# Optimization experiments

Hardware: AMD Instinct MI355X
Metric: run time of the kernel (lower is better)

## Reference

```python
import jax, jax.numpy as jnp
import numpy as np

N_NODES = 100000
N_EDGES = 1600000
D_IN = 64
D_OUT = 64


def setup_inputs() -> dict:
    key = jax.random.key(0)
    k1, k2, k3, k4, k5, k6 = jax.random.split(key, 6)
    feat = jax.random.normal(k1, (N_NODES, D_IN), dtype=jnp.float32)
    src = jax.random.randint(k2, (N_EDGES,), 0, N_NODES, dtype=jnp.int64)
    dst = jax.random.randint(k3, (N_EDGES,), 0, N_NODES, dtype=jnp.int64)
    edge_weight = jax.random.uniform(k4, (N_EDGES,), dtype=jnp.float32)
    # Xavier-uniform with relu gain, as in reset_parameters
    gain = float(np.sqrt(2.0))
    bound = gain * float(np.sqrt(6.0 / (D_IN + D_OUT)))
    W_neigh = jax.random.uniform(k5, (D_OUT, D_IN), dtype=jnp.float32, minval=-bound, maxval=bound)
    W_self = jax.random.uniform(k6, (D_OUT, D_IN), dtype=jnp.float32, minval=-bound, maxval=bound)
    bias = jnp.zeros((D_OUT,), dtype=jnp.float32)
    return {"feat": feat, "src": src, "dst": dst, "edge_weight": edge_weight,
            "W_neigh": W_neigh, "W_self": W_self, "bias": bias}


def reference(feat, src, dst, edge_weight, W_neigh, W_self, bias):
    n = feat.shape[0]
    # feat_drop with p=0.0 is identity; in_feats == out_feats so lin_before_mp is False
    # message: u_mul_e -> gather src features, scale by edge weight  [E, D_IN]
    m = feat[src] * edge_weight[:, None]
    # mean reduce over incoming edges (zero for isolated dst nodes, matching DGL)
    s = jax.ops.segment_sum(m, dst, num_segments=n)
    deg = jax.ops.segment_sum(jnp.ones_like(edge_weight), dst, num_segments=n)
    neigh = s / jnp.maximum(deg, 1.0)[:, None]
    h_neigh = neigh @ W_neigh.T
    h_self = feat @ W_self.T
    return h_self + h_neigh + bias
```

## Files before the change

kernel.cpp:

```cpp
#include <hip/hip_runtime.h>

constexpr int N_NODES = 100000;
constexpr int N_EDGES = 1600000;
constexpr int D = 64;

constexpr int BSH    = 6;
constexpr int BN     = 1 << BSH;
constexpr int NBUCK  = (N_NODES + BN - 1) / BN;
constexpr int NPART  = 400;
constexpr int EPB    = N_EDGES / NPART;
constexpr int NCVT   = (N_NODES * D / 4) / 256;

constexpr size_t OFF_BCNT    = 0;
constexpr size_t OFF_CURSOR  = 8192;
constexpr size_t OFF_BSTART  = 16384;
constexpr size_t OFF_ENTRIES = 24576;
constexpr size_t OFF_W16     = 24576 + (size_t)N_EDGES * 8;
constexpr size_t OFF_FEAT16  = OFF_W16 + 32768;
constexpr size_t OFF_ENT2    = OFF_FEAT16 + (size_t)N_NODES * D * 2;
constexpr size_t OFF_NSTART  = OFF_ENT2 + (size_t)N_EDGES * 8;
constexpr size_t WS_NEEDED   = OFF_NSTART + ((size_t)NBUCK * BN + 1) * 4;

typedef short  bf16x8 __attribute__((ext_vector_type(8)));
typedef float  f32x4  __attribute__((ext_vector_type(4)));

__device__ __forceinline__ unsigned short f2bf(float f) {
    unsigned u = __float_as_uint(f);
    u += 0x7fffu + ((u >> 16) & 1u);
    return (unsigned short)(u >> 16);
}

__device__ __forceinline__ void split8(float4 p0, float4 p1, bf16x8& hi, bf16x8& lo) {
    float f[8] = {p0.x, p0.y, p0.z, p0.w, p1.x, p1.y, p1.z, p1.w};
#pragma unroll
    for (int i = 0; i < 8; ++i) {
        const unsigned short h = f2bf(f[i]);
        const float hf = __uint_as_float((unsigned)h << 16);
        hi[i] = (short)h;
        lo[i] = (short)f2bf(f[i] - hf);
    }
}

__global__ __launch_bounds__(256) void k_zero(int* __restrict__ bcnt) {
    int i = blockIdx.x * 256 + threadIdx.x;
    if (i < NBUCK) bcnt[i] = 0;
}

__global__ __launch_bounds__(256) void k_pre(const float4* __restrict__ feat4,
                                             unsigned short* __restrict__ feat16,
                                             const float* __restrict__ Wn,
                                             const float* __restrict__ Ws,
                                             unsigned short* __restrict__ W16,
                                             const int* __restrict__ dst,
                                             int* __restrict__ bcnt) {
    __shared__ int l[NBUCK];
    const int b   = blockIdx.x;
    const int tid = threadIdx.x;
    if (b < NCVT) {
        const int i = b * 256 + tid;
        float4 v = feat4[i];
        ushort4 o;
        o.x = f2bf(v.x); o.y = f2bf(v.y); o.z = f2bf(v.z); o.w = f2bf(v.w);
        *(ushort4*)&feat16[(size_t)i * 4] = o;
    } else if (b < NCVT + NPART) {
        const int base = (b - NCVT) * EPB;
        for (int i = tid; i < NBUCK; i += 256) l[i] = 0;
        __syncthreads();
        for (int k = tid; k < EPB; k += 256)
            atomicAdd(&l[dst[base + k] >> BSH], 1);
        __syncthreads();
        for (int i = tid; i < NBUCK; i += 256)
            if (l[i]) atomicAdd(&bcnt[i], l[i]);
    } else {
        for (int e = tid; e < D * 128; e += 256) {
            const int j = e >> 7, k = e & 127;
            const float w = (k < D) ? Ws[j * D + k] : Wn[j * D + (k - D)];
            const unsigned short h = f2bf(w);
            const float hf = __uint_as_float((unsigned)h << 16);
            W16[e] = h;
            W16[D * 128 + e] = f2bf(w - hf);
        }
    }
}

__global__ __launch_bounds__(1024) void k_scan(const int* __restrict__ bcnt,
                                               int* __restrict__ bstart,
                                               int* __restrict__ cursor) {
    __shared__ int s[1024];
    const int t  = threadIdx.x;
    const int i0 = 2 * t, i1 = 2 * t + 1;
    const int c0 = (i0 < NBUCK) ? bcnt[i0] : 0;
    const int c1 = (i1 < NBUCK) ? bcnt[i1] : 0;
    const int v  = c0 + c1;
    s[t] = v;
    __syncthreads();
    for (int off = 1; off < 1024; off <<= 1) {
        int u = (t >= off) ? s[t - off] : 0;
        __syncthreads();
        s[t] += u;
        __syncthreads();
    }
    const int excl = s[t] - v;
    if (i0 < NBUCK) { bstart[i0] = excl;      cursor[i0] = excl; }
    if (i1 < NBUCK) { bstart[i1] = excl + c0; cursor[i1] = excl + c0; }
    if (t == 0) bstart[NBUCK] = N_EDGES;
}

__global__ __launch_bounds__(256) void k_part(const int* __restrict__ src,
                                              const int* __restrict__ dst,
                                              const float* __restrict__ ew,
                                              int* __restrict__ cursor,
                                              uint2* __restrict__ entries) {
    __shared__ int l[NBUCK];
    const int tid  = threadIdx.x;
    const int base = blockIdx.x * EPB;
    for (int i = tid; i < NBUCK; i += 256) l[i] = 0;
    __syncthreads();
    for (int k = tid; k < EPB; k += 256)
        atomicAdd(&l[dst[base + k] >> BSH], 1);
    __syncthreads();
    for (int b = tid; b < NBUCK; b += 256) {
        const int c = l[b];
        l[b] = c ? atomicAdd(&cursor[b], c) : 0;
    }
    __syncthreads();
    for (int k = tid; k < EPB; k += 256) {
        const int e = base + k;
        const int d = dst[e];
        const int pos = atomicAdd(&l[d >> BSH], 1);
        entries[pos] = make_uint2((unsigned)src[e] | ((unsigned)(d & (BN - 1)) << 17),
                                  __float_as_uint(ew[e]));
    }
}

__global__ __launch_bounds__(256) void k_sort(const int* __restrict__ bstart,
                                              const uint2* __restrict__ entries,
                                              uint2* __restrict__ entries2,
                                              int* __restrict__ nstart) {
    __shared__ int hh[BN], st[BN], cur[BN];
    const int tid = threadIdx.x;
    const int b   = blockIdx.x;
    const int s0  = bstart[b];
    const int cnt = bstart[b + 1] - s0;

    if (tid < BN) hh[tid] = 0;
    __syncthreads();
    for (int i = tid; i < cnt; i += 256)
        atomicAdd(&hh[(entries[s0 + i].x >> 17) & (BN - 1)], 1);
    __syncthreads();
    if (tid < BN) st[tid] = hh[tid];
    __syncthreads();
    for (int off = 1; off < BN; off <<= 1) {
        int u = 0;
        if (tid < BN && tid >= off) u = st[tid - off];
        __syncthreads();
        if (tid < BN) st[tid] += u;
        __syncthreads();
    }
    if (tid < BN) {
        const int e0 = st[tid] - hh[tid];
        st[tid] = e0; cur[tid] = e0;
        nstart[b * BN + tid] = s0 + e0;
    }
    if (b == NBUCK - 1 && tid == 0) nstart[NBUCK * BN] = N_EDGES;
    __syncthreads();
    for (int i = tid; i < cnt; i += 256) {
        uint2 e = entries[s0 + i];
        const int pos = atomicAdd(&cur[(e.x >> 17) & (BN - 1)], 1);
        entries2[s0 + pos] = e;
    }
}

__global__ __launch_bounds__(256, 8) void k_bucket(
    const uint2* __restrict__ feat16u2,
    const float* __restrict__ feat32,
    const int* __restrict__ nstart,
    const uint2* __restrict__ entries2,
    const unsigned short* __restrict__ W16,
    const float* __restrict__ bias,
    float* __restrict__ out) {
    __shared__ __align__(16) float aggrow[BN * 68];
    __shared__ int hh[BN], st[BN];
    const int tid = threadIdx.x;
    const int b   = blockIdx.x;

    if (tid < BN) {
        const int s = nstart[b * BN + tid];
        const int e = nstart[b * BN + tid + 1];
        st[tid] = s;
        hh[tid] = e - s;
    }
    __syncthreads();

    const int wave = tid >> 6, lane = tid & 63;
    const int group = lane >> 4, gl = lane & 15;
    for (int t = 0; t < 16; ++t) {
        const int dl  = wave * 16 + t;
        const int ss  = st[dl];
        const int deg = hh[dl];
        const int se  = ss + deg;
        float4 acc = make_float4(0.f, 0.f, 0.f, 0.f);
        for (int e = ss + group; e < se; e += 4) {
            const uint2 en = entries2[e];
            const float w  = __uint_as_float(en.y);
            const uint2 p  = feat16u2[(size_t)(en.x & 0x1FFFF) * 16 + gl];
            acc.x = fmaf(__uint_as_float(p.x << 16),         w, acc.x);
            acc.y = fmaf(__uint_as_float(p.x & 0xFFFF0000u), w, acc.y);
            acc.z = fmaf(__uint_as_float(p.y << 16),         w, acc.z);
            acc.w = fmaf(__uint_as_float(p.y & 0xFFFF0000u), w, acc.w);
        }
#pragma unroll
        for (int m = 16; m <= 32; m <<= 1) {
            acc.x += __shfl_xor(acc.x, m);
            acc.y += __shfl_xor(acc.y, m);
            acc.z += __shfl_xor(acc.z, m);
            acc.w += __shfl_xor(acc.w, m);
        }
        if (group == 0) {
            const float inv = 1.0f / fmaxf((float)deg, 1.0f);
            float4 o = make_float4(acc.x * inv, acc.y * inv, acc.z * inv, acc.w * inv);
            *(float4*)&aggrow[dl * 68 + gl * 4] = o;
        }
    }
    __syncthreads();

    const int quad = lane >> 4, r = lane & 15;
    const int node0 = b * BN + wave * 16;
    int arow = node0 + r;
    if (arow > N_NODES - 1) arow = N_NODES - 1;

    bf16x8 ahi[4], alo[4];
    {
        const float* fp = &feat32[(size_t)arow * 64 + quad * 8];
        split8(*(const float4*)fp,        *(const float4*)(fp + 4),  ahi[0], alo[0]);
        split8(*(const float4*)(fp + 32), *(const float4*)(fp + 36), ahi[1], alo[1]);
        const float* ap = &aggrow[(wave * 16 + r) * 68 + quad * 8];
        split8(*(const float4*)ap,        *(const float4*)(ap + 4),  ahi[2], alo[2]);
        split8(*(const float4*)(ap + 32), *(const float4*)(ap + 36), ahi[3], alo[3]);
    }

    const unsigned short* W16lo = W16 + D * 128;
    f32x4 acc4[4] = {};
#pragma unroll
    for (int nt = 0; nt < 4; ++nt) {
#pragma unroll
        for (int kc = 0; kc < 4; ++kc) {
            const size_t wo = (size_t)(nt * 16 + r) * 128 + kc * 32 + quad * 8;
            const bf16x8 bhi = *(const bf16x8*)&W16[wo];
            const bf16x8 blo = *(const bf16x8*)&W16lo[wo];
            acc4[nt] = __builtin_amdgcn_mfma_f32_16x16x32_bf16(ahi[kc], bhi, acc4[nt], 0, 0, 0);
            acc4[nt] = __builtin_amdgcn_mfma_f32_16x16x32_bf16(alo[kc], bhi, acc4[nt], 0, 0, 0);
            acc4[nt] = __builtin_amdgcn_mfma_f32_16x16x32_bf16(ahi[kc], blo, acc4[nt], 0, 0, 0);
        }
    }

#pragma unroll
    for (int nt = 0; nt < 4; ++nt) {
        const float bv = bias[nt * 16 + r];
#pragma unroll
        for (int reg = 0; reg < 4; ++reg) {
            const int m = node0 + quad * 4 + reg;
            if (m < N_NODES) out[(size_t)m * 64 + nt * 16 + r] = acc4[nt][reg] + bv;
        }
    }
}

__global__ __launch_bounds__(256) void fb_zero(float4* __restrict__ out4,
                                               float* __restrict__ deg) {
    const int stride = gridDim.x * blockDim.x;
    int i = blockIdx.x * blockDim.x + threadIdx.x;
    const int total4 = (N_NODES * D) / 4;
    for (int idx = i; idx < total4; idx += stride)
        out4[idx] = make_float4(0.f, 0.f, 0.f, 0.f);
    for (int idx = i; idx < N_NODES; idx += stride)
        deg[idx] = 0.f;
}

__global__ __launch_bounds__(256) void fb_scatter(
    const float* __restrict__ feat, const int* __restrict__ src,
    const int* __restrict__ dst, const float* __restrict__ ew,
    float* __restrict__ out, float* __restrict__ deg) {
    const int gid  = blockIdx.x * blockDim.x + threadIdx.x;
    const int e    = gid >> 6;
    const int lane = gid & 63;
    if (e >= N_EDGES) return;
    atomicAdd(&out[(size_t)dst[e] * D + lane], feat[(size_t)src[e] * D + lane] * ew[e]);
    if (lane == 0) atomicAdd(&deg[dst[e]], 1.0f);
}

__global__ __launch_bounds__(256) void fb_finalize(
    const float* __restrict__ feat, const float* __restrict__ Wn,
    const float* __restrict__ Ws, const float* __restrict__ bias,
    const float* __restrict__ deg, float* __restrict__ out) {
    __shared__ float lWn[D * 65];
    __shared__ float lWs[D * 65];
    for (int idx = threadIdx.x; idx < D * D; idx += 256) {
        const int r = idx >> 6, c = idx & 63;
        lWn[r * 65 + c] = Wn[idx];
        lWs[r * 65 + c] = Ws[idx];
    }
    __syncthreads();
    const int wave = threadIdx.x >> 6;
    const int lane = threadIdx.x & 63;
    const int n = blockIdx.x * 4 + wave;
    if (n >= N_NODES) return;
    const float f  = feat[(size_t)n * D + lane];
    const float sv = out[(size_t)n * D + lane];
    const float inv = 1.0f / fmaxf(deg[n], 1.0f);
    float acc_s = 0.f, acc_n = 0.f;
#pragma unroll
    for (int k = 0; k < D; ++k) {
        acc_s += __shfl(f, k)  * lWs[lane * 65 + k];
        acc_n += __shfl(sv, k) * lWn[lane * 65 + k];
    }
    out[(size_t)n * D + lane] = acc_s + acc_n * inv + bias[lane];
}

extern "C" void kernel_launch(void* const* d_in, const int* in_sizes, int n_in,
                              void* d_out, int out_size, void* d_ws, size_t ws_size,
                              hipStream_t stream) {
    const float* feat = (const float*)d_in[0];
    const int*   src  = (const int*)  d_in[1];
    const int*   dst  = (const int*)  d_in[2];
    const float* ew   = (const float*)d_in[3];
    const float* Wn   = (const float*)d_in[4];
    const float* Ws   = (const float*)d_in[5];
    const float* bias = (const float*)d_in[6];
    float* out = (float*)d_out;
    char* ws = (char*)d_ws;

    if (ws_size >= WS_NEEDED) {
        int*   bcnt    = (int*)(ws + OFF_BCNT);
        int*   cursor  = (int*)(ws + OFF_CURSOR);
        int*   bstart  = (int*)(ws + OFF_BSTART);
        uint2* entries = (uint2*)(ws + OFF_ENTRIES);
        unsigned short* W16    = (unsigned short*)(ws + OFF_W16);
        unsigned short* feat16 = (unsigned short*)(ws + OFF_FEAT16);
        uint2* entries2 = (uint2*)(ws + OFF_ENT2);
        int*   nstart   = (int*)(ws + OFF_NSTART);

        k_zero  <<<(NBUCK + 255) / 256, 256, 0, stream>>>(bcnt);
        k_pre   <<<NCVT + NPART + 1, 256, 0, stream>>>((const float4*)feat, feat16,
                                                       Wn, Ws, W16, dst, bcnt);
        k_scan  <<<1, 1024, 0, stream>>>(bcnt, bstart, cursor);
        k_part  <<<NPART, 256, 0, stream>>>(src, dst, ew, cursor, entries);
        k_sort  <<<NBUCK, 256, 0, stream>>>(bstart, entries, entries2, nstart);
        k_bucket<<<NBUCK, 256, 0, stream>>>((const uint2*)feat16, feat, nstart,
                                            entries2, W16, bias, out);
    } else {
        float* deg = (float*)d_ws;
        fb_zero<<<2048, 256, 0, stream>>>((float4*)out, deg);
        fb_scatter<<<(N_EDGES * 64) / 256, 256, 0, stream>>>(feat, src, dst, ew, out, deg);
        fb_finalize<<<(N_NODES + 3) / 4, 256, 0, stream>>>(feat, Wn, Ws, bias, deg, out);
    }
}
```

Before: 257.9 us.

## Replace two-level bucket sort with per-node counting sort via global atomics

The edge partitioning pipeline changes from bucket counting, partition, and an in-bucket sort to a direct per-node count, a single-block scan over all nodes, and one placement pass that uses global atomics on per-node cursors. This removes the k_part and k_sort kernels and the intermediate entries buffer, at the cost of many contended global atomics and a longer serial scan inside one block. The aggregation loop is also unrolled by two edges per group so that more gathers are in flight.

```diff
diff --git a/kernel.cpp b/kernel.cpp
--- a/kernel.cpp
+++ b/kernel.cpp
@@ -7,19 +7,19 @@
 constexpr int BSH    = 6;
 constexpr int BN     = 1 << BSH;
 constexpr int NBUCK  = (N_NODES + BN - 1) / BN;
-constexpr int NPART  = 400;
-constexpr int EPB    = N_EDGES / NPART;
+constexpr int NN2    = NBUCK * BN;
+constexpr int NCNTB  = 800;
+constexpr int EPB2   = N_EDGES / NCNTB;
 constexpr int NCVT   = (N_NODES * D / 4) / 256;
-
-constexpr size_t OFF_BCNT    = 0;
-constexpr size_t OFF_CURSOR  = 8192;
-constexpr size_t OFF_BSTART  = 16384;
-constexpr size_t OFF_ENTRIES = 24576;
-constexpr size_t OFF_W16     = 24576 + (size_t)N_EDGES * 8;
-constexpr size_t OFF_FEAT16  = OFF_W16 + 32768;
+constexpr int NPLACE = 1024;
+
+constexpr size_t OFF_NCNT    = 0;
+constexpr size_t OFF_NSTART  = 400384;
+constexpr size_t OFF_NCUR    = 800768;
+constexpr size_t OFF_W16     = 1201152;
+constexpr size_t OFF_FEAT16  = 1233920;
 constexpr size_t OFF_ENT2    = OFF_FEAT16 + (size_t)N_NODES * D * 2;
-constexpr size_t OFF_NSTART  = OFF_ENT2 + (size_t)N_EDGES * 8;
-constexpr size_t WS_NEEDED   = OFF_NSTART + ((size_t)NBUCK * BN + 1) * 4;
+constexpr size_t WS_NEEDED   = OFF_ENT2 + (size_t)N_EDGES * 8;
 
 typedef short  bf16x8 __attribute__((ext_vector_type(8)));
 typedef float  f32x4  __attribute__((ext_vector_type(4)));
@@ -41,9 +41,9 @@
     }
 }
 
-__global__ __launch_bounds__(256) void k_zero(int* __restrict__ bcnt) {
+__global__ __launch_bounds__(256) void k_zero(int* __restrict__ ncnt) {
     int i = blockIdx.x * 256 + threadIdx.x;
-    if (i < NBUCK) bcnt[i] = 0;
+    if (i < NN2) ncnt[i] = 0;
 }
 
 __global__ __launch_bounds__(256) void k_pre(const float4* __restrict__ feat4,
@@ -52,8 +52,7 @@
                                              const float* __restrict__ Ws,
                                              unsigned short* __restrict__ W16,
                                              const int* __restrict__ dst,
-                                             int* __restrict__ bcnt) {
-    __shared__ int l[NBUCK];
+                                             int* __restrict__ ncnt) {
     const int b   = blockIdx.x;
     const int tid = threadIdx.x;
     if (b < NCVT) {
@@ -62,15 +61,10 @@
         ushort4 o;
         o.x = f2bf(v.x); o.y = f2bf(v.y); o.z = f2bf(v.z); o.w = f2bf(v.w);
         *(ushort4*)&feat16[(size_t)i * 4] = o;
-    } else if (b < NCVT + NPART) {
-        const int base = (b - NCVT) * EPB;
-        for (int i = tid; i < NBUCK; i += 256) l[i] = 0;
-        __syncthreads();
-        for (int k = tid; k < EPB; k += 256)
-            atomicAdd(&l[dst[base + k] >> BSH], 1);
-        __syncthreads();
-        for (int i = tid; i < NBUCK; i += 256)
-            if (l[i]) atomicAdd(&bcnt[i], l[i]);
+    } else if (b < NCVT + NCNTB) {
+        const int base = (b - NCVT) * EPB2;
+        for (int k = tid; k < EPB2; k += 256)
+            atomicAdd(&ncnt[dst[base + k]], 1);
     } else {
         for (int e = tid; e < D * 128; e += 256) {
             const int j = e >> 7, k = e & 127;
@@ -83,16 +77,19 @@
     }
 }
 
-__global__ __launch_bounds__(1024) void k_scan(const int* __restrict__ bcnt,
-                                               int* __restrict__ bstart,
-                                               int* __restrict__ cursor) {
+constexpr int SCAN_PER = (NN2 + 1 + 1023) / 1024;
+__global__ __launch_bounds__(1024) void k_nscan(const int* __restrict__ ncnt,
+                                                int* __restrict__ nstart,
+                                                int* __restrict__ ncur) {
     __shared__ int s[1024];
-    const int t  = threadIdx.x;
-    const int i0 = 2 * t, i1 = 2 * t + 1;
-    const int c0 = (i0 < NBUCK) ? bcnt[i0] : 0;
-    const int c1 = (i1 < NBUCK) ? bcnt[i1] : 0;
-    const int v  = c0 + c1;
-    s[t] = v;
+    const int t    = threadIdx.x;
+    const int base = t * SCAN_PER;
+    int sum = 0;
+    for (int j = 0; j < SCAN_PER; ++j) {
+        const int idx = base + j;
+        sum += (idx < NN2) ? ncnt[idx] : 0;
+    }
+    s[t] = sum;
     __syncthreads();
     for (int off = 1; off < 1024; off <<= 1) {
         int u = (t >= off) ? s[t - off] : 0;
@@ -100,74 +97,26 @@
         s[t] += u;
         __syncthreads();
     }
-    const int excl = s[t] - v;
-    if (i0 < NBUCK) { bstart[i0] = excl;      cursor[i0] = excl; }
-    if (i1 < NBUCK) { bstart[i1] = excl + c0; cursor[i1] = excl + c0; }
-    if (t == 0) bstart[NBUCK] = N_EDGES;
-}
-
-__global__ __launch_bounds__(256) void k_part(const int* __restrict__ src,
-                                              const int* __restrict__ dst,
-                                              const float* __restrict__ ew,
-                                              int* __restrict__ cursor,
-                                              uint2* __restrict__ entries) {
-    __shared__ int l[NBUCK];
-    const int tid  = threadIdx.x;
-    const int base = blockIdx.x * EPB;
-    for (int i = tid; i < NBUCK; i += 256) l[i] = 0;
-    __syncthreads();
-    for (int k = tid; k < EPB; k += 256)
-        atomicAdd(&l[dst[base + k] >> BSH], 1);
-    __syncthreads();
-    for (int b = tid; b < NBUCK; b += 256) {
-        const int c = l[b];
-        l[b] = c ? atomicAdd(&cursor[b], c) : 0;
-    }
-    __syncthreads();
-    for (int k = tid; k < EPB; k += 256) {
-        const int e = base + k;
-        const int d = dst[e];
-        const int pos = atomicAdd(&l[d >> BSH], 1);
-        entries[pos] = make_uint2((unsigned)src[e] | ((unsigned)(d & (BN - 1)) << 17),
-                                  __float_as_uint(ew[e]));
-    }
-}
-
-__global__ __launch_bounds__(256) void k_sort(const int* __restrict__ bstart,
-                                              const uint2* __restrict__ entries,
-                                              uint2* __restrict__ entries2,
-                                              int* __restrict__ nstart) {
-    __shared__ int hh[BN], st[BN], cur[BN];
-    const int tid = threadIdx.x;
-    const int b   = blockIdx.x;
-    const int s0  = bstart[b];
-    const int cnt = bstart[b + 1] - s0;
-
-    if (tid < BN) hh[tid] = 0;
-    __syncthreads();
-    for (int i = tid; i < cnt; i += 256)
-        atomicAdd(&hh[(entries[s0 + i].x >> 17) & (BN - 1)], 1);
-    __syncthreads();
-    if (tid < BN) st[tid] = hh[tid];
-    __syncthreads();
-    for (int off = 1; off < BN; off <<= 1) {
-        int u = 0;
-        if (tid < BN && tid >= off) u = st[tid - off];
-        __syncthreads();
-        if (tid < BN) st[tid] += u;
-        __syncthreads();
-    }
-    if (tid < BN) {
-        const int e0 = st[tid] - hh[tid];
-        st[tid] = e0; cur[tid] = e0;
-        nstart[b * BN + tid] = s0 + e0;
-    }
-    if (b == NBUCK - 1 && tid == 0) nstart[NBUCK * BN] = N_EDGES;
-    __syncthreads();
-    for (int i = tid; i < cnt; i += 256) {
-        uint2 e = entries[s0 + i];
-        const int pos = atomicAdd(&cur[(e.x >> 17) & (BN - 1)], 1);
-        entries2[s0 + pos] = e;
+    int run = s[t] - sum;
+    for (int j = 0; j < SCAN_PER; ++j) {
+        const int idx = base + j;
+        if (idx <= NN2) {
+            nstart[idx] = run;
+            if (idx < NN2) { ncur[idx] = run; run += ncnt[idx]; }
+        }
+    }
+}
+
+__global__ __launch_bounds__(256) void k_place(const int* __restrict__ src,
+                                               const int* __restrict__ dst,
+                                               const float* __restrict__ ew,
+                                               int* __restrict__ ncur,
+                                               uint2* __restrict__ entries2) {
+    const int stride = gridDim.x * 256;
+    for (int e = blockIdx.x * 256 + threadIdx.x; e < N_EDGES; e += stride) {
+        const int d   = dst[e];
+        const int pos = atomicAdd(&ncur[d], 1);
+        entries2[pos] = make_uint2((unsigned)src[e], __float_as_uint(ew[e]));
     }
 }
 
@@ -200,10 +149,27 @@
         const int deg = hh[dl];
         const int se  = ss + deg;
         float4 acc = make_float4(0.f, 0.f, 0.f, 0.f);
-        for (int e = ss + group; e < se; e += 4) {
+        int e = ss + group;
+        for (; e + 4 < se; e += 8) {
+            const uint2 en0 = entries2[e];
+            const uint2 en1 = entries2[e + 4];
+            const uint2 p0  = feat16u2[(size_t)en0.x * 16 + gl];
+            const uint2 p1  = feat16u2[(size_t)en1.x * 16 + gl];
+            const float w0  = __uint_as_float(en0.y);
+            const float w1  = __uint_as_float(en1.y);
+            acc.x = fmaf(__uint_as_float(p0.x << 16),         w0, acc.x);
+            acc.y = fmaf(__uint_as_float(p0.x & 0xFFFF0000u), w0, acc.y);
+            acc.z = fmaf(__uint_as_float(p0.y << 16),         w0, acc.z);
+            acc.w = fmaf(__uint_as_float(p0.y & 0xFFFF0000u), w0, acc.w);
+            acc.x = fmaf(__uint_as_float(p1.x << 16),         w1, acc.x);
+            acc.y = fmaf(__uint_as_float(p1.x & 0xFFFF0000u), w1, acc.y);
+            acc.z = fmaf(__uint_as_float(p1.y << 16),         w1, acc.z);
+            acc.w = fmaf(__uint_as_float(p1.y & 0xFFFF0000u), w1, acc.w);
+        }
+        if (e < se) {
             const uint2 en = entries2[e];
             const float w  = __uint_as_float(en.y);
-            const uint2 p  = feat16u2[(size_t)(en.x & 0x1FFFF) * 16 + gl];
+            const uint2 p  = feat16u2[(size_t)en.x * 16 + gl];
             acc.x = fmaf(__uint_as_float(p.x << 16),         w, acc.x);
             acc.y = fmaf(__uint_as_float(p.x & 0xFFFF0000u), w, acc.y);
             acc.z = fmaf(__uint_as_float(p.y << 16),         w, acc.z);
@@ -330,21 +296,18 @@
     char* ws = (char*)d_ws;
 
     if (ws_size >= WS_NEEDED) {
-        int*   bcnt    = (int*)(ws + OFF_BCNT);
-        int*   cursor  = (int*)(ws + OFF_CURSOR);
-        int*   bstart  = (int*)(ws + OFF_BSTART);
-        uint2* entries = (uint2*)(ws + OFF_ENTRIES);
+        int* ncnt   = (int*)(ws + OFF_NCNT);
+        int* nstart = (int*)(ws + OFF_NSTART);
+        int* ncur   = (int*)(ws + OFF_NCUR);
         unsigned short* W16    = (unsigned short*)(ws + OFF_W16);
         unsigned short* feat16 = (unsigned short*)(ws + OFF_FEAT16);
         uint2* entries2 = (uint2*)(ws + OFF_ENT2);
-        int*   nstart   = (int*)(ws + OFF_NSTART);
-
-        k_zero  <<<(NBUCK + 255) / 256, 256, 0, stream>>>(bcnt);
-        k_pre   <<<NCVT + NPART + 1, 256, 0, stream>>>((const float4*)feat, feat16,
-                                                       Wn, Ws, W16, dst, bcnt);
-        k_scan  <<<1, 1024, 0, stream>>>(bcnt, bstart, cursor);
-        k_part  <<<NPART, 256, 0, stream>>>(src, dst, ew, cursor, entries);
-        k_sort  <<<NBUCK, 256, 0, stream>>>(bstart, entries, entries2, nstart);
+
+        k_zero  <<<(NN2 + 255) / 256, 256, 0, stream>>>(ncnt);
+        k_pre   <<<NCVT + NCNTB + 1, 256, 0, stream>>>((const float4*)feat, feat16,
+                                                       Wn, Ws, W16, dst, ncnt);
+        k_nscan <<<1, 1024, 0, stream>>>(ncnt, nstart, ncur);
+        k_place <<<NPLACE, 256, 0, stream>>>(src, dst, ew, ncur, entries2);
         k_bucket<<<NBUCK, 256, 0, stream>>>((const uint2*)feat16, feat, nstart,
                                             entries2, W16, bias, out);
     } else {
```

Result: slower. 609.9 us (+136.5%).
